# Optimization experiments

Hardware: AMD Instinct MI355X
Metric: run time of the kernel (lower is better)

The kernel has to match this reference:

```python
import jax, jax.numpy as jnp
import numpy as np

FP8_MAX = 448.0  # max finite value of float8_e4m3fn

M, K, N = 16384, 4096, 4096


def setup_inputs() -> dict:
    key = jax.random.key(0)
    kx, kw = jax.random.split(key)
    x = jax.random.normal(kx, (M, K), dtype=jnp.float32)
    w = jax.random.normal(kw, (K, N), dtype=jnp.float32)
    return {"x": x, "w": w}


def _quantize_e4m3(t, scale):
    # fp32 math, clamp to fp8 range, then round-to-nearest via dtype cast
    q = jnp.clip(t * scale, -FP8_MAX, FP8_MAX)
    return q.astype(jnp.float8_e4m3fn)


def reference(x, w):
    # per-tensor absmax scales (matches absmax_atomic_kernel + scale = fp8_max/absmax)
    sx = FP8_MAX / jnp.max(jnp.abs(x))
    sw = FP8_MAX / jnp.max(jnp.abs(w))
    # quantize activation [M,K] and transposed weight [N,K] to fp8 e4m3
    xq = _quantize_e4m3(x, sx)                # [M,K] fp8
    wq_t = _quantize_e4m3(w.T, sw)            # [N,K] fp8 (transpose_quantize kernel)
    # scaled fp8 matmul with fp32 accumulation, dequantize by combined scale
    y = jnp.einsum("mk,nk->mn", xq.astype(jnp.float32), wq_t.astype(jnp.float32))
    return (y / (sx * sw)).astype(x.dtype)
```

## Files before the change

kernel.cpp:

```cpp
#include <hip/hip_runtime.h>

#define FP8_MAX 448.0f

typedef float f32x4 __attribute__((ext_vector_type(4)));

__device__ __forceinline__ void load_lds16(const void* g, void* l) {
  __builtin_amdgcn_global_load_lds(
      (__attribute__((address_space(1))) void*)g,
      (__attribute__((address_space(3))) void*)l,
      16, 0, 0);
}

__global__ void init_scales_kernel(unsigned* s) {
  s[0] = 0u;
  s[1] = 0u;
}

__global__ void absmax_kernel(const float4* __restrict__ in,
                              unsigned* __restrict__ out, int n4) {
  float m = 0.f;
  int stride = gridDim.x * blockDim.x;
  for (int i = blockIdx.x * blockDim.x + threadIdx.x; i < n4; i += stride) {
    float4 v = in[i];
    m = fmaxf(m, fmaxf(fmaxf(fabsf(v.x), fabsf(v.y)),
                       fmaxf(fabsf(v.z), fabsf(v.w))));
  }
#pragma unroll
  for (int off = 32; off > 0; off >>= 1)
    m = fmaxf(m, __shfl_down(m, off, 64));
  __shared__ float sred[4];
  int lane = threadIdx.x & 63;
  int wid = threadIdx.x >> 6;
  if (lane == 0) sred[wid] = m;
  __syncthreads();
  if (threadIdx.x == 0) {
    m = fmaxf(fmaxf(sred[0], sred[1]), fmaxf(sred[2], sred[3]));
    atomicMax(out, __float_as_uint(m));
  }
}

__global__ void quant_x_kernel(const float* __restrict__ x,
                               unsigned char* __restrict__ xq,
                               const unsigned* __restrict__ sc, long long n16) {
  long long t = (long long)blockIdx.x * blockDim.x + threadIdx.x;
  if (t >= n16) return;
  float s = FP8_MAX / __uint_as_float(sc[0]);
  const float4* xv = (const float4*)x + t * 4;
  unsigned r[4];
#pragma unroll
  for (int i = 0; i < 4; ++i) {
    float4 v = xv[i];
    float q0 = fminf(fmaxf(v.x * s, -FP8_MAX), FP8_MAX);
    float q1 = fminf(fmaxf(v.y * s, -FP8_MAX), FP8_MAX);
    float q2 = fminf(fmaxf(v.z * s, -FP8_MAX), FP8_MAX);
    float q3 = fminf(fmaxf(v.w * s, -FP8_MAX), FP8_MAX);
    int p = __builtin_amdgcn_cvt_pk_fp8_f32(q0, q1, 0, false);
    p = __builtin_amdgcn_cvt_pk_fp8_f32(q2, q3, p, true);
    r[i] = (unsigned)p;
  }
  uint4 o;
  o.x = r[0]; o.y = r[1]; o.z = r[2]; o.w = r[3];
  *(uint4*)(xq + t * 16) = o;
}

__global__ void quant_wt_kernel(const float* __restrict__ w,
                                unsigned char* __restrict__ wq,
                                const unsigned* __restrict__ sc, int K, int N) {
  __shared__ float tile[64][65];
  float s = FP8_MAX / __uint_as_float(sc[1]);
  int nt = blockIdx.x * 64;
  int kt = blockIdx.y * 64;
#pragma unroll
  for (int it = 0; it < 4; ++it) {
    int idx = threadIdx.x + it * 256;
    int r = idx >> 4;
    int c = (idx & 15) * 4;
    float4 v = *(const float4*)&w[(size_t)(kt + r) * N + nt + c];
    tile[r][c + 0] = v.x; tile[r][c + 1] = v.y;
    tile[r][c + 2] = v.z; tile[r][c + 3] = v.w;
  }
  __syncthreads();
  int n = threadIdx.x >> 2;
  int k0 = (threadIdx.x & 3) * 16;
  unsigned r4[4];
#pragma unroll
  for (int q = 0; q < 4; ++q) {
    float a0 = fminf(fmaxf(tile[k0 + q * 4 + 0][n] * s, -FP8_MAX), FP8_MAX);
    float a1 = fminf(fmaxf(tile[k0 + q * 4 + 1][n] * s, -FP8_MAX), FP8_MAX);
    float a2 = fminf(fmaxf(tile[k0 + q * 4 + 2][n] * s, -FP8_MAX), FP8_MAX);
    float a3 = fminf(fmaxf(tile[k0 + q * 4 + 3][n] * s, -FP8_MAX), FP8_MAX);
    int p = __builtin_amdgcn_cvt_pk_fp8_f32(a0, a1, 0, false);
    p = __builtin_amdgcn_cvt_pk_fp8_f32(a2, a3, p, true);
    r4[q] = (unsigned)p;
  }
  uint4 o;
  o.x = r4[0]; o.y = r4[1]; o.z = r4[2]; o.w = r4[3];
  *(uint4*)&wq[(size_t)(nt + n) * K + kt + k0] = o;
}

__global__ __launch_bounds__(256) void gemm_fp8_kernel(
    const unsigned char* __restrict__ A,
    const unsigned char* __restrict__ B,
    float* __restrict__ C,
    const unsigned* __restrict__ am, int M, int N, int K) {
  __shared__ unsigned char lA[128 * 64];
  __shared__ unsigned char lB[128 * 64];

  const int tid = threadIdx.x;
  const int lane = tid & 63;
  const int wave = tid >> 6;
  const int wm = (wave >> 1) * 64;
  const int wn = (wave & 1) * 64;
  const int quad = lane >> 4;
  const int l16 = lane & 15;

  const int m0 = blockIdx.y * 128;
  const int n0 = blockIdx.x * 128;

  f32x4 zero4 = {0.f, 0.f, 0.f, 0.f};
  f32x4 acc[4][4];
#pragma unroll
  for (int i = 0; i < 4; ++i)
#pragma unroll
    for (int j = 0; j < 4; ++j) acc[i][j] = zero4;

  const int row0 = tid >> 2;
  const int c0 = tid & 3;
  const int sc0 = c0 ^ ((row0 >> 1) & 3);
  const int row1 = row0 + 64;
  const unsigned char* gA0 = A + (size_t)(m0 + row0) * K + sc0 * 16;
  const unsigned char* gA1 = A + (size_t)(m0 + row1) * K + sc0 * 16;
  const unsigned char* gB0 = B + (size_t)(n0 + row0) * K + sc0 * 16;
  const unsigned char* gB1 = B + (size_t)(n0 + row1) * K + sc0 * 16;
  unsigned char* sA0 = &lA[tid * 16];
  unsigned char* sA1 = &lA[(tid + 256) * 16];
  unsigned char* sB0 = &lB[tid * 16];
  unsigned char* sB1 = &lB[(tid + 256) * 16];

  int aoff[2][4], boff[2][4];
#pragma unroll
  for (int s = 0; s < 2; ++s)
#pragma unroll
    for (int i = 0; i < 4; ++i) {
      int chunk = s * 2 + (quad >> 1);
      int mrow = wm + i * 16 + l16;
      int nrow = wn + i * 16 + l16;
      aoff[s][i] = mrow * 64 + (chunk ^ ((mrow >> 1) & 3)) * 16 + (quad & 1) * 8;
      boff[s][i] = nrow * 64 + (chunk ^ ((nrow >> 1) & 3)) * 16 + (quad & 1) * 8;
    }

  for (int k0 = 0; k0 < K; k0 += 64) {
    load_lds16(gA0 + k0, sA0);
    load_lds16(gA1 + k0, sA1);
    load_lds16(gB0 + k0, sB0);
    load_lds16(gB1 + k0, sB1);
    __syncthreads();
#pragma unroll
    for (int s = 0; s < 2; ++s) {
      long long af[4], bf[4];
#pragma unroll
      for (int i = 0; i < 4; ++i) {
        af[i] = *(const long long*)&lA[aoff[s][i]];
        bf[i] = *(const long long*)&lB[boff[s][i]];
      }
#pragma unroll
      for (int i = 0; i < 4; ++i)
#pragma unroll
        for (int j = 0; j < 4; ++j)
          acc[i][j] = __builtin_amdgcn_mfma_f32_16x16x32_fp8_fp8(
              af[i], bf[j], acc[i][j], 0, 0, 0);
    }
    __syncthreads();
  }

  float ax = __uint_as_float(am[0]);
  float aw = __uint_as_float(am[1]);
  float sx = FP8_MAX / ax;
  float sw = FP8_MAX / aw;
  float inv = 1.f / (sx * sw);

#pragma unroll
  for (int i = 0; i < 4; ++i) {
    int crow = m0 + wm + i * 16 + quad * 4;
#pragma unroll
    for (int j = 0; j < 4; ++j) {
      int ccol = n0 + wn + j * 16 + l16;
#pragma unroll
      for (int r = 0; r < 4; ++r)
        C[(size_t)(crow + r) * N + ccol] = acc[i][j][r] * inv;
    }
  }
}

extern "C" void kernel_launch(void* const* d_in, const int* in_sizes, int n_in,
                              void* d_out, int out_size, void* d_ws,
                              size_t ws_size, hipStream_t stream) {
  const int M = 16384, K = 4096, N = 4096;
  const float* x = (const float*)d_in[0];
  const float* w = (const float*)d_in[1];
  float* out = (float*)d_out;

  unsigned* scales = (unsigned*)d_ws;
  unsigned char* xq = (unsigned char*)d_ws + 256;
  unsigned char* wq = xq + (size_t)M * K;

  init_scales_kernel<<<1, 1, 0, stream>>>(scales);
  absmax_kernel<<<8192, 256, 0, stream>>>((const float4*)x, scales + 0, M * K / 4);
  absmax_kernel<<<2048, 256, 0, stream>>>((const float4*)w, scales + 1, K * N / 4);
  quant_x_kernel<<<(M * (long long)K / 16 + 255) / 256, 256, 0, stream>>>(
      x, xq, scales, (long long)M * K / 16);
  quant_wt_kernel<<<dim3(N / 64, K / 64), 256, 0, stream>>>(w, wq, scales, K, N);
  gemm_fp8_kernel<<<dim3(N / 128, M / 128), 256, 0, stream>>>(xq, wq, out,
                                                              scales, M, N, K);
}
```

Baseline: 1.003 ms.

## Switch GEMM to 32x32x64 scaled FP8 MFMA and simplify x quantization

The GEMM inner loop now uses the gfx950 mfma_scale 32x32x64 f8f6f4 instruction with unit scales instead of 16x16x32 fp8 MFMAs. This cuts MFMA issue count and lets each lane read 16-byte LDS fragments. The LDS swizzle and epilogue row mapping change to match the new operand and accumulator layout. The x quantization kernel is also reworked so each thread handles one float4 and writes 4 bytes, trading wider per-thread stores for more threads.

```diff
diff --git a/kernel.cpp b/kernel.cpp
--- a/kernel.cpp
+++ b/kernel.cpp
@@ -2,7 +2,9 @@
 
 #define FP8_MAX 448.0f
 
-typedef float f32x4 __attribute__((ext_vector_type(4)));
+typedef float f32x16 __attribute__((ext_vector_type(16)));
+typedef int v8i __attribute__((ext_vector_type(8)));
+typedef int v4i __attribute__((ext_vector_type(4)));
 
 __device__ __forceinline__ void load_lds16(const void* g, void* l) {
   __builtin_amdgcn_global_load_lds(
@@ -39,28 +41,20 @@
   }
 }
 
-__global__ void quant_x_kernel(const float* __restrict__ x,
-                               unsigned char* __restrict__ xq,
-                               const unsigned* __restrict__ sc, long long n16) {
-  long long t = (long long)blockIdx.x * blockDim.x + threadIdx.x;
-  if (t >= n16) return;
+__global__ void quant_x_kernel(const float4* __restrict__ x,
+                               unsigned* __restrict__ xq,
+                               const unsigned* __restrict__ sc, int n4) {
+  int t = blockIdx.x * blockDim.x + threadIdx.x;
+  if (t >= n4) return;
   float s = FP8_MAX / __uint_as_float(sc[0]);
-  const float4* xv = (const float4*)x + t * 4;
-  unsigned r[4];
-#pragma unroll
-  for (int i = 0; i < 4; ++i) {
-    float4 v = xv[i];
-    float q0 = fminf(fmaxf(v.x * s, -FP8_MAX), FP8_MAX);
-    float q1 = fminf(fmaxf(v.y * s, -FP8_MAX), FP8_MAX);
-    float q2 = fminf(fmaxf(v.z * s, -FP8_MAX), FP8_MAX);
-    float q3 = fminf(fmaxf(v.w * s, -FP8_MAX), FP8_MAX);
-    int p = __builtin_amdgcn_cvt_pk_fp8_f32(q0, q1, 0, false);
-    p = __builtin_amdgcn_cvt_pk_fp8_f32(q2, q3, p, true);
-    r[i] = (unsigned)p;
-  }
-  uint4 o;
-  o.x = r[0]; o.y = r[1]; o.z = r[2]; o.w = r[3];
-  *(uint4*)(xq + t * 16) = o;
+  float4 v = x[t];
+  float q0 = fminf(fmaxf(v.x * s, -FP8_MAX), FP8_MAX);
+  float q1 = fminf(fmaxf(v.y * s, -FP8_MAX), FP8_MAX);
+  float q2 = fminf(fmaxf(v.z * s, -FP8_MAX), FP8_MAX);
+  float q3 = fminf(fmaxf(v.w * s, -FP8_MAX), FP8_MAX);
+  int p = __builtin_amdgcn_cvt_pk_fp8_f32(q0, q1, 0, false);
+  p = __builtin_amdgcn_cvt_pk_fp8_f32(q2, q3, p, true);
+  xq[t] = (unsigned)p;
 }
 
 __global__ void quant_wt_kernel(const float* __restrict__ w,
@@ -111,22 +105,22 @@
   const int wave = tid >> 6;
   const int wm = (wave >> 1) * 64;
   const int wn = (wave & 1) * 64;
-  const int quad = lane >> 4;
-  const int l16 = lane & 15;
+  const int l31 = lane & 31;
+  const int kh = lane >> 5;
 
   const int m0 = blockIdx.y * 128;
   const int n0 = blockIdx.x * 128;
 
-  f32x4 zero4 = {0.f, 0.f, 0.f, 0.f};
-  f32x4 acc[4][4];
-#pragma unroll
-  for (int i = 0; i < 4; ++i)
-#pragma unroll
-    for (int j = 0; j < 4; ++j) acc[i][j] = zero4;
+  f32x16 acc[2][2];
+#pragma unroll
+  for (int i = 0; i < 2; ++i)
+#pragma unroll
+    for (int j = 0; j < 2; ++j)
+#pragma unroll
+      for (int r = 0; r < 16; ++r) acc[i][j][r] = 0.f;
 
   const int row0 = tid >> 2;
-  const int c0 = tid & 3;
-  const int sc0 = c0 ^ ((row0 >> 1) & 3);
+  const int sc0 = (tid & 3) ^ (row0 & 3);
   const int row1 = row0 + 64;
   const unsigned char* gA0 = A + (size_t)(m0 + row0) * K + sc0 * 16;
   const unsigned char* gA1 = A + (size_t)(m0 + row1) * K + sc0 * 16;
@@ -137,17 +131,18 @@
   unsigned char* sB0 = &lB[tid * 16];
   unsigned char* sB1 = &lB[(tid + 256) * 16];
 
-  int aoff[2][4], boff[2][4];
-#pragma unroll
-  for (int s = 0; s < 2; ++s)
-#pragma unroll
-    for (int i = 0; i < 4; ++i) {
-      int chunk = s * 2 + (quad >> 1);
-      int mrow = wm + i * 16 + l16;
-      int nrow = wn + i * 16 + l16;
-      aoff[s][i] = mrow * 64 + (chunk ^ ((mrow >> 1) & 3)) * 16 + (quad & 1) * 8;
-      boff[s][i] = nrow * 64 + (chunk ^ ((nrow >> 1) & 3)) * 16 + (quad & 1) * 8;
-    }
+  int aoff[2][2], boff[2][2];
+#pragma unroll
+  for (int sub = 0; sub < 2; ++sub) {
+    int ra = wm + sub * 32 + l31;
+    int fa = ra & 3;
+    aoff[sub][0] = ra * 64 + ((kh * 2 + 0) ^ fa) * 16;
+    aoff[sub][1] = ra * 64 + ((kh * 2 + 1) ^ fa) * 16;
+    int rb = wn + sub * 32 + l31;
+    int fb = rb & 3;
+    boff[sub][0] = rb * 64 + ((kh * 2 + 0) ^ fb) * 16;
+    boff[sub][1] = rb * 64 + ((kh * 2 + 1) ^ fb) * 16;
+  }
 
   for (int k0 = 0; k0 < K; k0 += 64) {
     load_lds16(gA0 + k0, sA0);
@@ -155,21 +150,27 @@
     load_lds16(gB0 + k0, sB0);
     load_lds16(gB1 + k0, sB1);
     __syncthreads();
-#pragma unroll
-    for (int s = 0; s < 2; ++s) {
-      long long af[4], bf[4];
-#pragma unroll
-      for (int i = 0; i < 4; ++i) {
-        af[i] = *(const long long*)&lA[aoff[s][i]];
-        bf[i] = *(const long long*)&lB[boff[s][i]];
-      }
-#pragma unroll
-      for (int i = 0; i < 4; ++i)
-#pragma unroll
-        for (int j = 0; j < 4; ++j)
-          acc[i][j] = __builtin_amdgcn_mfma_f32_16x16x32_fp8_fp8(
-              af[i], bf[j], acc[i][j], 0, 0, 0);
+
+    v8i af[2], bf[2];
+#pragma unroll
+    for (int sub = 0; sub < 2; ++sub) {
+      v4i alo = *(const v4i*)&lA[aoff[sub][0]];
+      v4i ahi = *(const v4i*)&lA[aoff[sub][1]];
+      af[sub] = __builtin_shufflevector(alo, ahi, 0, 1, 2, 3, 4, 5, 6, 7);
+      v4i blo = *(const v4i*)&lB[boff[sub][0]];
+      v4i bhi = *(const v4i*)&lB[boff[sub][1]];
+      bf[sub] = __builtin_shufflevector(blo, bhi, 0, 1, 2, 3, 4, 5, 6, 7);
     }
+#pragma unroll
+    for (int si = 0; si < 2; ++si)
+#pragma unroll
+      for (int sj = 0; sj < 2; ++sj)
+        acc[si][sj] = __builtin_amdgcn_mfma_scale_f32_32x32x64_f8f6f4(
+            af[si], bf[sj], acc[si][sj],
+            0, 0,
+            0, 0x7f7f7f7f,
+            0, 0x7f7f7f7f);
+
     __syncthreads();
   }
 
@@ -180,16 +181,16 @@
   float inv = 1.f / (sx * sw);
 
 #pragma unroll
-  for (int i = 0; i < 4; ++i) {
-    int crow = m0 + wm + i * 16 + quad * 4;
-#pragma unroll
-    for (int j = 0; j < 4; ++j) {
-      int ccol = n0 + wn + j * 16 + l16;
-#pragma unroll
-      for (int r = 0; r < 4; ++r)
-        C[(size_t)(crow + r) * N + ccol] = acc[i][j][r] * inv;
+  for (int si = 0; si < 2; ++si)
+#pragma unroll
+    for (int sj = 0; sj < 2; ++sj) {
+      int colbase = n0 + wn + sj * 32 + l31;
+#pragma unroll
+      for (int r = 0; r < 16; ++r) {
+        int row = m0 + wm + si * 32 + (r & 3) + 8 * (r >> 2) + 4 * kh;
+        C[(size_t)row * N + colbase] = acc[si][sj][r] * inv;
+      }
     }
-  }
 }
 
 extern "C" void kernel_launch(void* const* d_in, const int* in_sizes, int n_in,
@@ -205,11 +206,14 @@
   unsigned char* wq = xq + (size_t)M * K;
 
   init_scales_kernel<<<1, 1, 0, stream>>>(scales);
-  absmax_kernel<<<8192, 256, 0, stream>>>((const float4*)x, scales + 0, M * K / 4);
-  absmax_kernel<<<2048, 256, 0, stream>>>((const float4*)w, scales + 1, K * N / 4);
-  quant_x_kernel<<<(M * (long long)K / 16 + 255) / 256, 256, 0, stream>>>(
-      x, xq, scales, (long long)M * K / 16);
-  quant_wt_kernel<<<dim3(N / 64, K / 64), 256, 0, stream>>>(w, wq, scales, K, N);
+  absmax_kernel<<<8192, 256, 0, stream>>>((const float4*)x, scales + 0,
+                                          M * K / 4);
+  absmax_kernel<<<2048, 256, 0, stream>>>((const float4*)w, scales + 1,
+                                          K * N / 4);
+  quant_x_kernel<<<(M * K / 4 + 255) / 256, 256, 0, stream>>>(
+      (const float4*)x, (unsigned*)xq, scales, M * K / 4);
+  quant_wt_kernel<<<dim3(N / 64, K / 64), 256, 0, stream>>>(w, wq, scales, K,
+                                                            N);
   gemm_fp8_kernel<<<dim3(N / 128, M / 128), 256, 0, stream>>>(xq, wq, out,
                                                               scales, M, N, K);
 }
```

After: 923.2 us. 1.09x faster.
